# Kernel optimization log

Hardware: AMD Instinct MI355X
Metric: run time of the kernel (lower is better)

The kernel has to match this reference:

```python
import jax, jax.numpy as jnp
import numpy as np

HIDDEN = 128
AUG = 2          # aug_dim
SUBSTEPS = 2     # fixed dopri5 substeps per output interval (replaces adaptive stepping)
B = 16384
T = 8


def _xavier(key, shape, gain=5.0 / 3.0):
    fan_in, fan_out = shape
    lim = gain * np.sqrt(6.0 / (fan_in + fan_out))
    return jax.random.uniform(key, shape, jnp.float32, -lim, lim)


def setup_inputs() -> dict:
    key = jax.random.key(0)
    ks = jax.random.split(key, 4)
    return {
        "r0": jax.random.normal(ks[0], (B, 2), jnp.float32),
        "t": jnp.linspace(0.0, 1.0, T, dtype=jnp.float32),
        "W1": _xavier(ks[1], (5, HIDDEN)),
        "b1": jnp.zeros((HIDDEN,), jnp.float32),
        "W2": _xavier(ks[2], (HIDDEN, HIDDEN)),
        "b2": jnp.zeros((HIDDEN,), jnp.float32),
        "W3": _xavier(ks[3], (HIDDEN, 2)),
        "b3": jnp.zeros((2,), jnp.float32),
    }


def _ode_f(t, s, W1, b1, W2, b2, W3, b3):
    # s: [B, 2+AUG]; t: scalar -> concat time feature, tiny tanh MLP
    tf = t * jnp.ones((s.shape[0], 1), s.dtype)
    inp = jnp.concatenate([s, tf], axis=-1)            # [B, 5]
    h = jnp.tanh(inp @ W1 + b1)                        # [B, 128]
    h = jnp.tanh(h @ W2 + b2)                          # [B, 128]
    v_xy = h @ W3 + b3                                 # [B, 2]
    v_a = jnp.zeros((s.shape[0], AUG), s.dtype)        # static aug dynamics
    return jnp.concatenate([v_xy, v_a], axis=-1)


def _dopri5_step(f, t, s, dt):
    # Dormand-Prince RK45 tableau, 5th-order solution advance (as torchdiffeq dopri5)
    k1 = f(t, s)
    k2 = f(t + dt * (1.0 / 5.0), s + dt * (1.0 / 5.0) * k1)
    k3 = f(t + dt * (3.0 / 10.0), s + dt * ((3.0 / 40.0) * k1 + (9.0 / 40.0) * k2))
    k4 = f(t + dt * (4.0 / 5.0),
           s + dt * ((44.0 / 45.0) * k1 - (56.0 / 15.0) * k2 + (32.0 / 9.0) * k3))
    k5 = f(t + dt * (8.0 / 9.0),
           s + dt * ((19372.0 / 6561.0) * k1 - (25360.0 / 2187.0) * k2
                     + (64448.0 / 6561.0) * k3 - (212.0 / 729.0) * k4))
    k6 = f(t + dt,
           s + dt * ((9017.0 / 3168.0) * k1 - (355.0 / 33.0) * k2
                     + (46732.0 / 5247.0) * k3 + (49.0 / 176.0) * k4
                     - (5103.0 / 18656.0) * k5))
    return s + dt * ((35.0 / 384.0) * k1 + (500.0 / 1113.0) * k3
                     + (125.0 / 192.0) * k4 - (2187.0 / 6784.0) * k5
                     + (11.0 / 84.0) * k6)


def _integrate(r0, t, W1, b1, W2, b2, W3, b3):
    s0 = jnp.concatenate([r0, jnp.zeros((r0.shape[0], AUG), r0.dtype)], axis=-1)
    f = lambda tt, ss: _ode_f(tt, ss, W1, b1, W2, b2, W3, b3)

    def interval(s, ts):
        t0, t1 = ts
        dt = (t1 - t0) / SUBSTEPS
        for j in range(SUBSTEPS):  # small fixed loop, unrolled
            s = _dopri5_step(f, t0 + j * dt, s, dt)
        return s, s

    _, ys = jax.lax.scan(interval, s0, (t[:-1], t[1:]))   # [T-1, B, 4]
    traj = jnp.concatenate([s0[None], ys], axis=0)        # [T, B, 4]
    return jnp.transpose(traj, (1, 0, 2))[..., :2]        # [B, T, 2]


def reference(r0, t, W1, b1, W2, b2, W3, b3):
    return _integrate(r0, t, W1, b1, W2, b2, W3, b3)
```

## Files before the change

### kernel.cpp

```cpp
#include <hip/hip_runtime.h>


#define HID 128
#define TT  8
#define F(a,b) ((float)((double)(a)/(double)(b)))
#define K2C 2.8853900817779268f

typedef __attribute__((ext_vector_type(8))) short bf16x8;
typedef __attribute__((ext_vector_type(4))) float f32x4;
typedef __attribute__((ext_vector_type(2))) float f32x2;

union Frag { bf16x8 v; unsigned short u[8]; unsigned int d[4]; };

__device__ __forceinline__ f32x2 bc(float s) { return f32x2{s, s}; }
__device__ __forceinline__ f32x2 pk_fma(f32x2 a, f32x2 b, f32x2 c) {
#if __has_builtin(__builtin_elementwise_fma)
  return __builtin_elementwise_fma(a, b, c);
#else
  return a * b + c;
#endif
}
__device__ __forceinline__ float exp2_fast(float x) {
#if __has_builtin(__builtin_amdgcn_exp2f)
  return __builtin_amdgcn_exp2f(x);
#else
  return __builtin_exp2f(x);
#endif
}
__device__ __forceinline__ unsigned short f2bf(float f) {
  unsigned u = __builtin_bit_cast(unsigned, f);
  u += 0x7FFFu + ((u >> 16) & 1u);
  return (unsigned short)(u >> 16);
}
__device__ __forceinline__ unsigned pack2bf(float a, float b) {
  unsigned ua = __builtin_bit_cast(unsigned, a);
  unsigned ub = __builtin_bit_cast(unsigned, b);
  ua += 0x7FFFu + ((ua >> 16) & 1u);
  ub += 0x7FFFu + ((ub >> 16) & 1u);
  return __builtin_amdgcn_perm(ub, ua, 0x07060302u);
}
__device__ __forceinline__ f32x2 tanh_pre(f32x2 u) {
  f32x2 e;
  e.x = exp2_fast(u.x);
  e.y = exp2_fast(u.y);
  f32x2 d = e + bc(1.0f);
  f32x2 r;
  r.x = __builtin_amdgcn_rcpf(d.x);
  r.y = __builtin_amdgcn_rcpf(d.y);
  return pk_fma(bc(-2.0f), r, bc(1.0f));
}

__global__ __launch_bounds__(64, 1) void node_kernel(
    const float* __restrict__ r0, const float* __restrict__ tarr,
    const float* __restrict__ W1, const float* __restrict__ b1,
    const float* __restrict__ W2, const float* __restrict__ b2,
    const float* __restrict__ W3, const float* __restrict__ b3,
    float* __restrict__ out)
{
  const int lane = (int)(threadIdx.x & 63u);
  const int quad = lane >> 4;
  const int m16  = lane & 15;
  const int s    = (int)blockIdx.x * 16 + m16;

  f32x2 w1x[16], w1y[16], w1t[16], bb1[16];
  #pragma unroll
  for (int kk = 0; kk < 4; ++kk)
    #pragma unroll
    for (int p = 0; p < 4; ++p) {
      int i = kk * 32 + quad * 8 + 2 * p;
      int idx = kk * 4 + p;
      w1x[idx] = f32x2{W1[0 * HID + i], W1[0 * HID + i + 1]} * bc(K2C);
      w1y[idx] = f32x2{W1[1 * HID + i], W1[1 * HID + i + 1]} * bc(K2C);
      w1t[idx] = f32x2{W1[4 * HID + i], W1[4 * HID + i + 1]} * bc(K2C);
      bb1[idx] = f32x2{b1[i], b1[i + 1]} * bc(K2C);
    }
  Frag W2f[8][4];
  #pragma unroll
  for (int t = 0; t < 8; ++t) {
    int o = t * 16 + m16;
    #pragma unroll
    for (int kk = 0; kk < 4; ++kk) {
      #pragma unroll
      for (int j = 0; j < 8; ++j)
        W2f[t][kk].u[j] = f2bf(W2[(kk * 32 + quad * 8 + j) * HID + o] * K2C);
      asm volatile("" : "+a"(W2f[t][kk].v));
    }
  }
  f32x4 b2i[8];
  f32x2 w3v[8][4];
  #pragma unroll
  for (int t = 0; t < 8; ++t) {
    #pragma unroll
    for (int rr = 0; rr < 4; ++rr) {
      int o = t * 16 + quad * 4 + rr;
      b2i[t][rr] = b2[o] * K2C;
      w3v[t][rr] = f32x2{W3[o * 2 + 0], W3[o * 2 + 1]};
    }
    asm volatile("" : "+a"(b2i[t]));
  }
  const f32x2 b3v = f32x2{b3[0], b3[1]};

  f32x2 S = f32x2{r0[2 * s + 0], r0[2 * s + 1]};
  if (lane < 16) *(float2*)&out[(s * TT + 0) * 2] = make_float2(S.x, S.y);

  auto feval = [&](float tt, f32x2 st) -> f32x2 {
    const f32x2 sx = bc(st.x), sy = bc(st.y), tv = bc(tt);
    f32x4 acc[8];
    #pragma unroll
    for (int kk = 0; kk < 4; ++kk) {
      unsigned pd[4];
      #pragma unroll
      for (int p = 0; p < 4; ++p) {
        int idx = kk * 4 + p;
        f32x2 a = pk_fma(sx, w1x[idx], bb1[idx]);
        a = pk_fma(sy, w1y[idx], a);
        a = pk_fma(tv, w1t[idx], a);
        f32x2 h = tanh_pre(a);
        pd[p] = pack2bf(h.x, h.y);
      }
      Frag bv;
      bv.d[0] = pd[0]; bv.d[1] = pd[1]; bv.d[2] = pd[2]; bv.d[3] = pd[3];
      if (kk == 0) {
        #pragma unroll
        for (int t = 0; t < 8; ++t)
          acc[t] = __builtin_amdgcn_mfma_f32_16x16x32_bf16(
              W2f[t][0].v, bv.v, b2i[t], 0, 0, 0);
      } else {
        #pragma unroll
        for (int t = 0; t < 8; ++t)
          acc[t] = __builtin_amdgcn_mfma_f32_16x16x32_bf16(
              W2f[t][kk].v, bv.v, acc[t], 0, 0, 0);
      }
    }
    f32x2 vs = bc(0.f);
    #pragma unroll
    for (int t = 0; t < 8; ++t)
      #pragma unroll
      for (int p = 0; p < 2; ++p) {
        f32x2 av = f32x2{acc[t][2 * p], acc[t][2 * p + 1]};
        f32x2 h2 = tanh_pre(av);
        vs = pk_fma(bc(h2.x), w3v[t][2 * p + 0], vs);
        vs = pk_fma(bc(h2.y), w3v[t][2 * p + 1], vs);
      }
    float px = vs.x, py = vs.y;
    px += __shfl_xor(px, 16); px += __shfl_xor(px, 32);
    py += __shfl_xor(py, 16); py += __shfl_xor(py, 32);
    return f32x2{px, py} + b3v;
  };

  #pragma unroll 1
  for (int iv = 0; iv < TT - 1; ++iv) {
    float t0 = tarr[iv], t1 = tarr[iv + 1];
    float dt = (t1 - t0) * 0.5f;
    #pragma unroll 1
    for (int ss = 0; ss < 2; ++ss) {
      float tb = (ss == 0) ? t0 : (t0 + dt);
      const f32x2 dtv = bc(dt);
      f32x2 k1 = feval(tb, S);
      f32x2 k2 = feval(tb + dt * F(1,5), pk_fma(bc(dt * F(1,5)), k1, S));
      f32x2 a3 = pk_fma(bc(F(9,40)), k2, bc(F(3,40)) * k1);
      f32x2 k3 = feval(tb + dt * F(3,10), pk_fma(dtv, a3, S));
      f32x2 a4 = pk_fma(bc(F(44,45)), k1,
                 pk_fma(bc(-F(56,15)), k2, bc(F(32,9)) * k3));
      f32x2 k4 = feval(tb + dt * F(4,5), pk_fma(dtv, a4, S));
      f32x2 a5 = pk_fma(bc(F(19372,6561)), k1,
                 pk_fma(bc(-F(25360,2187)), k2,
                 pk_fma(bc(F(64448,6561)), k3, bc(-F(212,729)) * k4)));
      f32x2 k5 = feval(tb + dt * F(8,9), pk_fma(dtv, a5, S));
      f32x2 a6 = pk_fma(bc(F(9017,3168)), k1,
                 pk_fma(bc(-F(355,33)), k2,
                 pk_fma(bc(F(46732,5247)), k3,
                 pk_fma(bc(F(49,176)), k4, bc(-F(5103,18656)) * k5))));
      f32x2 k6 = feval(tb + dt, pk_fma(dtv, a6, S));
      f32x2 fin = pk_fma(bc(F(35,384)), k1,
                  pk_fma(bc(F(500,1113)), k3,
                  pk_fma(bc(F(125,192)), k4,
                  pk_fma(bc(-F(2187,6784)), k5, bc(F(11,84)) * k6))));
      S = pk_fma(dtv, fin, S);
    }
    if (lane < 16) *(float2*)&out[(s * TT + iv + 1) * 2] = make_float2(S.x, S.y);
  }
}

extern "C" void kernel_launch(void* const* d_in, const int* in_sizes, int n_in,
                              void* d_out, int out_size, void* d_ws, size_t ws_size,
                              hipStream_t stream) {
  const float* r0 = (const float*)d_in[0];
  const float* t  = (const float*)d_in[1];
  const float* W1 = (const float*)d_in[2];
  const float* b1 = (const float*)d_in[3];
  const float* W2 = (const float*)d_in[4];
  const float* b2 = (const float*)d_in[5];
  const float* W3 = (const float*)d_in[6];
  const float* b3 = (const float*)d_in[7];
  float* out = (float*)d_out;
  const int B = in_sizes[0] / 2;
  dim3 grid(B / 16), block(64);
  node_kernel<<<grid, block, 0, stream>>>(r0, t, W1, b1, W2, b2, W3, b3, out);
}
```

Measured before the change: 182.1 us.

## Split each 16-sample tile's MLP evaluation across two waves with LDS exchange

```diff
diff --git a/kernel.cpp b/kernel.cpp
--- a/kernel.cpp
+++ b/kernel.cpp
@@ -50,102 +50,126 @@
   return pk_fma(bc(-2.0f), r, bc(1.0f));
 }
 
-__global__ __launch_bounds__(64, 1) void node_kernel(
+__global__ __launch_bounds__(128, 2) void node_kernel(
     const float* __restrict__ r0, const float* __restrict__ tarr,
     const float* __restrict__ W1, const float* __restrict__ b1,
     const float* __restrict__ W2, const float* __restrict__ b2,
     const float* __restrict__ W3, const float* __restrict__ b3,
     float* __restrict__ out)
 {
-  const int lane = (int)(threadIdx.x & 63u);
+  __shared__ uint4  h1X[16][16];
+  __shared__ float2 vpX[2][16];
+
+  const int tid  = (int)threadIdx.x;
+  const int lane = tid & 63;
+  const int w    = __builtin_amdgcn_readfirstlane(tid >> 6);
   const int quad = lane >> 4;
   const int m16  = lane & 15;
   const int s    = (int)blockIdx.x * 16 + m16;
-
-  f32x2 w1x[16], w1y[16], w1t[16], bb1[16];
+  const int ko   = (1 - w) * 2;
+
+  f32x2 w1x[8], w1y[8], w1t[8], bb1[8];
   #pragma unroll
-  for (int kk = 0; kk < 4; ++kk)
+  for (int so = 0; so < 2; ++so)
     #pragma unroll
     for (int p = 0; p < 4; ++p) {
-      int i = kk * 32 + quad * 8 + 2 * p;
-      int idx = kk * 4 + p;
+      int i = (2 * w + so) * 32 + quad * 8 + 2 * p;
+      int idx = so * 4 + p;
       w1x[idx] = f32x2{W1[0 * HID + i], W1[0 * HID + i + 1]} * bc(K2C);
       w1y[idx] = f32x2{W1[1 * HID + i], W1[1 * HID + i + 1]} * bc(K2C);
       w1t[idx] = f32x2{W1[4 * HID + i], W1[4 * HID + i + 1]} * bc(K2C);
       bb1[idx] = f32x2{b1[i], b1[i + 1]} * bc(K2C);
     }
-  Frag W2f[8][4];
+  Frag W2f[4][4];
   #pragma unroll
-  for (int t = 0; t < 8; ++t) {
-    int o = t * 16 + m16;
+  for (int tl = 0; tl < 4; ++tl) {
+    int o = (4 * w + tl) * 16 + m16;
     #pragma unroll
     for (int kk = 0; kk < 4; ++kk) {
       #pragma unroll
       for (int j = 0; j < 8; ++j)
-        W2f[t][kk].u[j] = f2bf(W2[(kk * 32 + quad * 8 + j) * HID + o] * K2C);
-      asm volatile("" : "+a"(W2f[t][kk].v));
+        W2f[tl][kk].u[j] = f2bf(W2[(kk * 32 + quad * 8 + j) * HID + o] * K2C);
+      asm volatile("" : "+a"(W2f[tl][kk].v));
     }
   }
-  f32x4 b2i[8];
-  f32x2 w3v[8][4];
+  f32x4 b2i[4];
+  f32x2 w3v[4][4];
   #pragma unroll
-  for (int t = 0; t < 8; ++t) {
+  for (int tl = 0; tl < 4; ++tl) {
     #pragma unroll
     for (int rr = 0; rr < 4; ++rr) {
-      int o = t * 16 + quad * 4 + rr;
-      b2i[t][rr] = b2[o] * K2C;
-      w3v[t][rr] = f32x2{W3[o * 2 + 0], W3[o * 2 + 1]};
-    }
-    asm volatile("" : "+a"(b2i[t]));
+      int o = (4 * w + tl) * 16 + quad * 4 + rr;
+      b2i[tl][rr] = b2[o] * K2C;
+      w3v[tl][rr] = f32x2{W3[o * 2 + 0], W3[o * 2 + 1]};
+    }
+    asm volatile("" : "+a"(b2i[tl]));
   }
   const f32x2 b3v = f32x2{b3[0], b3[1]};
 
   f32x2 S = f32x2{r0[2 * s + 0], r0[2 * s + 1]};
-  if (lane < 16) *(float2*)&out[(s * TT + 0) * 2] = make_float2(S.x, S.y);
+  if (tid < 16) *(float2*)&out[(s * TT + 0) * 2] = make_float2(S.x, S.y);
 
   auto feval = [&](float tt, f32x2 st) -> f32x2 {
     const f32x2 sx = bc(st.x), sy = bc(st.y), tv = bc(tt);
-    f32x4 acc[8];
-    #pragma unroll
-    for (int kk = 0; kk < 4; ++kk) {
+    uint4 own[2];
+    #pragma unroll
+    for (int so = 0; so < 2; ++so) {
       unsigned pd[4];
       #pragma unroll
       for (int p = 0; p < 4; ++p) {
-        int idx = kk * 4 + p;
+        int idx = so * 4 + p;
         f32x2 a = pk_fma(sx, w1x[idx], bb1[idx]);
         a = pk_fma(sy, w1y[idx], a);
         a = pk_fma(tv, w1t[idx], a);
         f32x2 h = tanh_pre(a);
         pd[p] = pack2bf(h.x, h.y);
       }
-      Frag bv;
-      bv.d[0] = pd[0]; bv.d[1] = pd[1]; bv.d[2] = pd[2]; bv.d[3] = pd[3];
-      if (kk == 0) {
-        #pragma unroll
-        for (int t = 0; t < 8; ++t)
-          acc[t] = __builtin_amdgcn_mfma_f32_16x16x32_bf16(
-              W2f[t][0].v, bv.v, b2i[t], 0, 0, 0);
-      } else {
-        #pragma unroll
-        for (int t = 0; t < 8; ++t)
-          acc[t] = __builtin_amdgcn_mfma_f32_16x16x32_bf16(
-              W2f[t][kk].v, bv.v, acc[t], 0, 0, 0);
-      }
-    }
-    f32x2 vs = bc(0.f);
-    #pragma unroll
-    for (int t = 0; t < 8; ++t)
+      own[so] = make_uint4(pd[0], pd[1], pd[2], pd[3]);
+      h1X[(2 * w + so) * 4 + quad][m16] = own[so];
+    }
+    __syncthreads();
+    uint4 q0 = h1X[(ko + 0) * 4 + quad][m16];
+    uint4 q1 = h1X[(ko + 1) * 4 + quad][m16];
+    Frag bv;
+    f32x4 acc[4];
+    bv.d[0] = own[0].x; bv.d[1] = own[0].y; bv.d[2] = own[0].z; bv.d[3] = own[0].w;
+    #pragma unroll
+    for (int tl = 0; tl < 4; ++tl)
+      acc[tl] = __builtin_amdgcn_mfma_f32_16x16x32_bf16(
+          W2f[tl][2 * w].v, bv.v, b2i[tl], 0, 0, 0);
+    bv.d[0] = own[1].x; bv.d[1] = own[1].y; bv.d[2] = own[1].z; bv.d[3] = own[1].w;
+    #pragma unroll
+    for (int tl = 0; tl < 4; ++tl)
+      acc[tl] = __builtin_amdgcn_mfma_f32_16x16x32_bf16(
+          W2f[tl][2 * w + 1].v, bv.v, acc[tl], 0, 0, 0);
+    bv.d[0] = q0.x; bv.d[1] = q0.y; bv.d[2] = q0.z; bv.d[3] = q0.w;
+    #pragma unroll
+    for (int tl = 0; tl < 4; ++tl)
+      acc[tl] = __builtin_amdgcn_mfma_f32_16x16x32_bf16(
+          W2f[tl][ko].v, bv.v, acc[tl], 0, 0, 0);
+    bv.d[0] = q1.x; bv.d[1] = q1.y; bv.d[2] = q1.z; bv.d[3] = q1.w;
+    #pragma unroll
+    for (int tl = 0; tl < 4; ++tl)
+      acc[tl] = __builtin_amdgcn_mfma_f32_16x16x32_bf16(
+          W2f[tl][ko + 1].v, bv.v, acc[tl], 0, 0, 0);
+    f32x2 vsa[2] = {bc(0.f), bc(0.f)};
+    #pragma unroll
+    for (int tl = 0; tl < 4; ++tl)
       #pragma unroll
       for (int p = 0; p < 2; ++p) {
-        f32x2 av = f32x2{acc[t][2 * p], acc[t][2 * p + 1]};
+        f32x2 av = f32x2{acc[tl][2 * p], acc[tl][2 * p + 1]};
         f32x2 h2 = tanh_pre(av);
-        vs = pk_fma(bc(h2.x), w3v[t][2 * p + 0], vs);
-        vs = pk_fma(bc(h2.y), w3v[t][2 * p + 1], vs);
+        vsa[tl & 1] = pk_fma(bc(h2.x), w3v[tl][2 * p + 0], vsa[tl & 1]);
+        vsa[tl & 1] = pk_fma(bc(h2.y), w3v[tl][2 * p + 1], vsa[tl & 1]);
       }
+    f32x2 vs = vsa[0] + vsa[1];
     float px = vs.x, py = vs.y;
-    px += __shfl_xor(px, 16); px += __shfl_xor(px, 32);
-    py += __shfl_xor(py, 16); py += __shfl_xor(py, 32);
-    return f32x2{px, py} + b3v;
+    px += __shfl_xor(px, 16); py += __shfl_xor(py, 16);
+    px += __shfl_xor(px, 32); py += __shfl_xor(py, 32);
+    if (lane < 16) vpX[w][m16] = make_float2(px, py);
+    __syncthreads();
+    float2 q = vpX[1 - w][m16];
+    return f32x2{px, py} + f32x2{q.x, q.y} + b3v;
   };
 
   #pragma unroll 1
@@ -178,7 +202,7 @@
                   pk_fma(bc(-F(2187,6784)), k5, bc(F(11,84)) * k6))));
       S = pk_fma(dtv, fin, S);
     }
-    if (lane < 16) *(float2*)&out[(s * TT + iv + 1) * 2] = make_float2(S.x, S.y);
+    if (tid < 16) *(float2*)&out[(s * TT + iv + 1) * 2] = make_float2(S.x, S.y);
   }
 }
 
@@ -195,6 +219,6 @@
   const float* b3 = (const float*)d_in[7];
   float* out = (float*)d_out;
   const int B = in_sizes[0] / 2;
-  dim3 grid(B / 16), block(64);
+  dim3 grid(B / 16), block(128);
   node_kernel<<<grid, block, 0, stream>>>(r0, t, W1, b1, W2, b2, W3, b3, out);
 }
```

Result: slower. 408.1 us (+124.1%).
